# Kernel optimization log

Hardware: AMD Instinct MI355X
Metric: run time of the kernel (lower is better)

Reference implementation:

```python
import jax, jax.numpy as jnp
import numpy as np

B, L, H = 8, 2048, 2048
N_ACTIONS = 8
NEG_INF = -1e30


def setup_inputs() -> dict:
    key = jax.random.key(0)
    k1, k2, k3, k4, k5 = jax.random.split(key, 5)
    stdv = 1.0 / np.sqrt(H)
    return {
        "x": jax.random.normal(k1, (B, L, H), dtype=jnp.float32),
        "y": jax.random.normal(k2, (B, H), dtype=jnp.float32),
        "x_mask": jnp.zeros((B, L), dtype=bool),
        "actions": jax.random.randint(k3, (B,), 0, N_ACTIONS),
        "weight": jax.random.uniform(k4, (H, H), jnp.float32, -stdv, stdv),  # [y_size, x_size]
        "bias": jnp.zeros((H,), dtype=jnp.float32),
        "wa": jax.random.uniform(k5, (N_ACTIONS, H, H), jnp.float32, -stdv, stdv),
        "ba": jnp.zeros((N_ACTIONS, H), dtype=jnp.float32),
    }


def reference(x, y, x_mask, actions, weight, bias, wa, ba):
    # Gather the per-sample action weights (math-identical to the original
    # compute-all-then-one-hot-select loop, without the O(n_actions) waste).
    wa_sel = wa[actions]                      # [B, h2, h1]
    ba_sel = ba[actions]                      # [B, h1]
    # func='mul_s': W_a = weight * sigmoid(wa[a]); b_a = bias * sigmoid(ba[a])
    W = weight[None, :, :] * jax.nn.sigmoid(wa_sel)   # [B, h2, h1]
    Wy = jnp.einsum('bh,bhx->bx', y, W) + bias[None, :] * jax.nn.sigmoid(ba_sel)  # [B, h1]
    xWy = jnp.einsum('blh,bh->bl', x, Wy)     # [B, L]
    xWy = jnp.where(x_mask, NEG_INF, xWy)
    # eval-mode path of the original (softmax); training uses log_softmax
    return jax.nn.softmax(xWy, axis=-1)
```

## Files before the change

### kernel.cpp

```cpp
#include <hip/hip_runtime.h>
#include <hip/hip_bf16.h>
#include <math.h>

#define B 8
#define L 2048
#define H 2048
#define NA 8
#define NEG_INF (-1e30f)

#define HCHUNKS 32
#define HC_SZ (H / HCHUNKS)

__device__ __forceinline__ float sigf(float t) {
    return 1.0f / (1.0f + __expf(-t));
}

__global__ __launch_bounds__(256) void k_wy_partial(
    const float* __restrict__ y, const int* __restrict__ actions,
    const float* __restrict__ weight, const float* __restrict__ wa,
    float* __restrict__ partial)
{
    const int bx = blockIdx.x;
    const int hc = blockIdx.y;
    const int b  = bx >> 1;
    const int x0 = (bx & 1) * 1024 + threadIdx.x * 4;
    const int a  = actions[b];
    const int h0 = hc * HC_SZ;

    const float* __restrict__ yb     = y + b * H;
    const float* __restrict__ wbase  = weight + (size_t)h0 * H + x0;
    const float* __restrict__ wabase = wa + ((size_t)a * H + h0) * H + x0;

    float4 acc = make_float4(0.f, 0.f, 0.f, 0.f);
    #pragma unroll 4
    for (int i = 0; i < HC_SZ; ++i) {
        const float  yv = yb[h0 + i];
        const float4 w4 = *(const float4*)(wbase  + (size_t)i * H);
        const float4 a4 = *(const float4*)(wabase + (size_t)i * H);
        acc.x += yv * w4.x * sigf(a4.x);
        acc.y += yv * w4.y * sigf(a4.y);
        acc.z += yv * w4.z * sigf(a4.z);
        acc.w += yv * w4.w * sigf(a4.w);
    }
    *(float4*)(partial + ((size_t)(b * HCHUNKS + hc) * H) + x0) = acc;
}

__global__ __launch_bounds__(256) void k_wy_reduce(
    const float* __restrict__ partial, const float* __restrict__ bias,
    const float* __restrict__ ba, const int* __restrict__ actions,
    float* __restrict__ Wy)
{
    const int idx = blockIdx.x * 256 + threadIdx.x;
    const int b   = idx / (H / 4);
    const int x0  = (idx % (H / 4)) * 4;
    const int a   = actions[b];

    float4 s = make_float4(0.f, 0.f, 0.f, 0.f);
    const float* __restrict__ p = partial + (size_t)b * HCHUNKS * H + x0;
    #pragma unroll 8
    for (int c = 0; c < HCHUNKS; ++c) {
        const float4 v = *(const float4*)(p + (size_t)c * H);
        s.x += v.x; s.y += v.y; s.z += v.z; s.w += v.w;
    }
    const float4 bi  = *(const float4*)(bias + x0);
    const float4 bav = *(const float4*)(ba + (size_t)a * H + x0);
    s.x += bi.x * sigf(bav.x);
    s.y += bi.y * sigf(bav.y);
    s.z += bi.z * sigf(bav.z);
    s.w += bi.w * sigf(bav.w);
    *(float4*)(Wy + (size_t)b * H + x0) = s;
}

__global__ __launch_bounds__(256) void k_xwy(
    const float* __restrict__ x, const float* __restrict__ Wy,
    const unsigned char* __restrict__ mask, float* __restrict__ xWy)
{
    const int wave = threadIdx.x >> 6;
    const int lane = threadIdx.x & 63;
    const int row  = blockIdx.x * 4 + wave;
    const int b    = row >> 11;

    const float* __restrict__ xb = x + (size_t)row * H;
    const float* __restrict__ wy = Wy + (size_t)b * H;

    float acc = 0.f;
    #pragma unroll
    for (int j = 0; j < H / 256; ++j) {
        const int off = j * 256 + lane * 4;
        const float4 xv = *(const float4*)(xb + off);
        const float4 wv = *(const float4*)(wy + off);
        acc += xv.x * wv.x + xv.y * wv.y + xv.z * wv.z + xv.w * wv.w;
    }
    #pragma unroll
    for (int s = 32; s; s >>= 1) acc += __shfl_xor(acc, s, 64);
    if (lane == 0) xWy[row] = mask[row] ? NEG_INF : acc;
}

__global__ __launch_bounds__(256) void k_softmax(
    const float* __restrict__ xWy, float* __restrict__ out)
{
    const int b    = blockIdx.x;
    const int tid  = threadIdx.x;
    const int wave = tid >> 6;
    const int lane = tid & 63;
    const float* __restrict__ v = xWy + (size_t)b * L;

    float vals[L / 256];
    float m = -INFINITY;
    #pragma unroll
    for (int j = 0; j < L / 256; ++j) {
        vals[j] = v[tid + j * 256];
        m = fmaxf(m, vals[j]);
    }
    #pragma unroll
    for (int s = 32; s; s >>= 1) m = fmaxf(m, __shfl_xor(m, s, 64));

    __shared__ float redm[4];
    if (lane == 0) redm[wave] = m;
    __syncthreads();
    m = fmaxf(fmaxf(redm[0], redm[1]), fmaxf(redm[2], redm[3]));

    float sum = 0.f;
    #pragma unroll
    for (int j = 0; j < L / 256; ++j) {
        vals[j] = __expf(vals[j] - m);
        sum += vals[j];
    }
    #pragma unroll
    for (int s = 32; s; s >>= 1) sum += __shfl_xor(sum, s, 64);

    __shared__ float reds[4];
    if (lane == 0) reds[wave] = sum;
    __syncthreads();
    sum = reds[0] + reds[1] + reds[2] + reds[3];

    const float inv = 1.0f / sum;
    #pragma unroll
    for (int j = 0; j < L / 256; ++j)
        out[(size_t)b * L + tid + j * 256] = vals[j] * inv;
}

extern "C" void kernel_launch(void* const* d_in, const int* in_sizes, int n_in,
                              void* d_out, int out_size, void* d_ws, size_t ws_size,
                              hipStream_t stream) {
    const float*         x       = (const float*)d_in[0];
    const float*         y       = (const float*)d_in[1];
    const unsigned char* mask    = (const unsigned char*)d_in[2];
    const int*           actions = (const int*)d_in[3];
    const float*         weight  = (const float*)d_in[4];
    const float*         bias    = (const float*)d_in[5];
    const float*         wa      = (const float*)d_in[6];
    const float*         ba      = (const float*)d_in[7];
    float*               out     = (float*)d_out;

    float* ws      = (float*)d_ws;
    float* partial = ws;
    float* Wy      = partial + (size_t)B * HCHUNKS * H;
    float* xWy     = Wy + (size_t)B * H;

    dim3 g1(B * 2, HCHUNKS);
    k_wy_partial<<<g1, 256, 0, stream>>>(y, actions, weight, wa, partial);
    k_wy_reduce<<<(B * H / 4) / 256, 256, 0, stream>>>(partial, bias, ba, actions, Wy);
    k_xwy<<<B * L / 4, 256, 0, stream>>>(x, Wy, mask, xWy);
    k_softmax<<<B, 256, 0, stream>>>(xWy, out);
}
```

Baseline: 60.32 us.

## Fuse Wy partial and reduce kernels with in-block LDS reduction; stage Wy in LDS

Merges the two-kernel Wy computation into a single kernel. Each block now covers 32 output columns across all of H and reduces its partial sums through shared memory, which removes the partial-sum buffer round-trip and one kernel launch. The y vector is staged in LDS, and the xWy kernel also loads Wy into LDS once per block. The new Wy kernel launches 512 blocks instead of 512 plus the reduce grid, and each thread reads only 16-byte strips of weight and wa rows, which may hurt coalescing.

```diff
diff --git a/kernel.cpp b/kernel.cpp
--- a/kernel.cpp
+++ b/kernel.cpp
@@ -8,67 +8,67 @@
 #define NA 8
 #define NEG_INF (-1e30f)
 
-#define HCHUNKS 32
-#define HC_SZ (H / HCHUNKS)
+#define XT 64
+#define COLS 32
 
 __device__ __forceinline__ float sigf(float t) {
     return 1.0f / (1.0f + __expf(-t));
 }
 
-__global__ __launch_bounds__(256) void k_wy_partial(
+__global__ __launch_bounds__(256) void k_wy(
     const float* __restrict__ y, const int* __restrict__ actions,
     const float* __restrict__ weight, const float* __restrict__ wa,
-    float* __restrict__ partial)
+    const float* __restrict__ bias, const float* __restrict__ ba,
+    float* __restrict__ Wy)
 {
-    const int bx = blockIdx.x;
-    const int hc = blockIdx.y;
-    const int b  = bx >> 1;
-    const int x0 = (bx & 1) * 1024 + threadIdx.x * 4;
+    const int b  = blockIdx.y;
+    const int x0 = blockIdx.x * COLS;
     const int a  = actions[b];
-    const int h0 = hc * HC_SZ;
+    const int c4 = threadIdx.x & 7;
+    const int hg = threadIdx.x >> 3;
 
-    const float* __restrict__ yb     = y + b * H;
-    const float* __restrict__ wbase  = weight + (size_t)h0 * H + x0;
-    const float* __restrict__ wabase = wa + ((size_t)a * H + h0) * H + x0;
+    __shared__ float ylds[H];
+    for (int i = threadIdx.x * 4; i < H; i += 1024)
+        *(float4*)(ylds + i) = *(const float4*)(y + (size_t)b * H + i);
+    __syncthreads();
+
+    const float* __restrict__ wp = weight + x0 + c4 * 4;
+    const float* __restrict__ ap = wa + (size_t)a * H * H + x0 + c4 * 4;
 
     float4 acc = make_float4(0.f, 0.f, 0.f, 0.f);
-    #pragma unroll 4
-    for (int i = 0; i < HC_SZ; ++i) {
-        const float  yv = yb[h0 + i];
-        const float4 w4 = *(const float4*)(wbase  + (size_t)i * H);
-        const float4 a4 = *(const float4*)(wabase + (size_t)i * H);
+    #pragma unroll 8
+    for (int h = hg; h < H; h += 32) {
+        const float  yv = ylds[h];
+        const float4 w4 = *(const float4*)(wp + (size_t)h * H);
+        const float4 a4 = *(const float4*)(ap + (size_t)h * H);
         acc.x += yv * w4.x * sigf(a4.x);
         acc.y += yv * w4.y * sigf(a4.y);
         acc.z += yv * w4.z * sigf(a4.z);
         acc.w += yv * w4.w * sigf(a4.w);
     }
-    *(float4*)(partial + ((size_t)(b * HCHUNKS + hc) * H) + x0) = acc;
-}
 
-__global__ __launch_bounds__(256) void k_wy_reduce(
-    const float* __restrict__ partial, const float* __restrict__ bias,
-    const float* __restrict__ ba, const int* __restrict__ actions,
-    float* __restrict__ Wy)
-{
-    const int idx = blockIdx.x * 256 + threadIdx.x;
-    const int b   = idx / (H / 4);
-    const int x0  = (idx % (H / 4)) * 4;
-    const int a   = actions[b];
+    __shared__ float4 red[32][8];
+    red[hg][c4] = acc;
+    __syncthreads();
+    #pragma unroll
+    for (int s = 16; s; s >>= 1) {
+        if (hg < s) {
+            const float4 v = red[hg + s][c4];
+            acc.x += v.x; acc.y += v.y; acc.z += v.z; acc.w += v.w;
+            red[hg][c4] = acc;
+        }
+        __syncthreads();
+    }
 
-    float4 s = make_float4(0.f, 0.f, 0.f, 0.f);
-    const float* __restrict__ p = partial + (size_t)b * HCHUNKS * H + x0;
-    #pragma unroll 8
-    for (int c = 0; c < HCHUNKS; ++c) {
-        const float4 v = *(const float4*)(p + (size_t)c * H);
-        s.x += v.x; s.y += v.y; s.z += v.z; s.w += v.w;
+    if (hg == 0) {
+        const float4 bi  = *(const float4*)(bias + x0 + c4 * 4);
+        const float4 bav = *(const float4*)(ba + (size_t)a * H + x0 + c4 * 4);
+        acc.x += bi.x * sigf(bav.x);
+        acc.y += bi.y * sigf(bav.y);
+        acc.z += bi.z * sigf(bav.z);
+        acc.w += bi.w * sigf(bav.w);
+        *(float4*)(Wy + (size_t)b * H + x0 + c4 * 4) = acc;
     }
-    const float4 bi  = *(const float4*)(bias + x0);
-    const float4 bav = *(const float4*)(ba + (size_t)a * H + x0);
-    s.x += bi.x * sigf(bav.x);
-    s.y += bi.y * sigf(bav.y);
-    s.z += bi.z * sigf(bav.z);
-    s.w += bi.w * sigf(bav.w);
-    *(float4*)(Wy + (size_t)b * H + x0) = s;
 }
 
 __global__ __launch_bounds__(256) void k_xwy(
@@ -78,17 +78,21 @@
     const int wave = threadIdx.x >> 6;
     const int lane = threadIdx.x & 63;
     const int row  = blockIdx.x * 4 + wave;
-    const int b    = row >> 11;
+    const int b    = (blockIdx.x * 4) >> 11;
+
+    __shared__ float wlds[H];
+    for (int i = threadIdx.x * 4; i < H; i += 1024)
+        *(float4*)(wlds + i) = *(const float4*)(Wy + (size_t)b * H + i);
+    __syncthreads();
 
     const float* __restrict__ xb = x + (size_t)row * H;
-    const float* __restrict__ wy = Wy + (size_t)b * H;
 
     float acc = 0.f;
     #pragma unroll
     for (int j = 0; j < H / 256; ++j) {
         const int off = j * 256 + lane * 4;
         const float4 xv = *(const float4*)(xb + off);
-        const float4 wv = *(const float4*)(wy + off);
+        const float4 wv = *(const float4*)(wlds + off);
         acc += xv.x * wv.x + xv.y * wv.y + xv.z * wv.z + xv.w * wv.w;
     }
     #pragma unroll
@@ -153,14 +157,12 @@
     const float*         ba      = (const float*)d_in[7];
     float*               out     = (float*)d_out;
 
-    float* ws      = (float*)d_ws;
-    float* partial = ws;
-    float* Wy      = partial + (size_t)B * HCHUNKS * H;
-    float* xWy     = Wy + (size_t)B * H;
+    float* ws  = (float*)d_ws;
+    float* Wy  = ws;
+    float* xWy = Wy + (size_t)B * H;
 
-    dim3 g1(B * 2, HCHUNKS);
-    k_wy_partial<<<g1, 256, 0, stream>>>(y, actions, weight, wa, partial);
-    k_wy_reduce<<<(B * H / 4) / 256, 256, 0, stream>>>(partial, bias, ba, actions, Wy);
+    dim3 g1(XT, B);
+    k_wy<<<g1, 256, 0, stream>>>(y, actions, weight, wa, bias, ba, Wy);
     k_xwy<<<B * L / 4, 256, 0, stream>>>(x, Wy, mask, xWy);
     k_softmax<<<B, 256, 0, stream>>>(xWy, out);
 }
```

Result: faster. 54.90 us (-9.0%).
